# Optimization experiments

Measured on AMD Instinct MI355X. Metric: run time of the kernel, lower is better.

The kernel has to match this reference:

```python
import jax, jax.numpy as jnp
import numpy as np

DIM = 128      # token feature dim
HEADS = 4
HEAD_DIM = DIM // HEADS
H = 512
W = 512
NSP = 4096     # n_spixels = H*W/scale
TEMP = DIM ** (-0.5)   # NOTE: original scales by full-dim ** -0.5
NEG = -9.0e15
EPS = 1e-12    # torch F.normalize eps


def setup_inputs() -> dict:
    key = jax.random.key(0)
    k1, k2, k3, k4 = jax.random.split(key, 4)
    return {
        "spf": jax.random.normal(k1, (DIM, NSP), jnp.float32),
        "segments": jax.random.randint(k2, (H, W), 0, NSP, jnp.int32),
        "w_qkv": jax.random.normal(k3, (DIM, 3 * DIM), jnp.float32) / np.sqrt(DIM),
        "w_out": jax.random.normal(k4, (DIM, DIM), jnp.float32) / np.sqrt(DIM),
        "b_out": jnp.zeros((DIM,), jnp.float32),
    }


def build_adjacency(seg, n_sp):
    """Vectorized version of get_A: for every 2x2 window (i in [0,h-3], j in [0,w-3])
    connect the max and min superpixel labels; zero the diagonal."""
    a = seg[:-2, :-2]
    b = seg[:-2, 1:-1]
    c = seg[1:-1, :-2]
    d = seg[1:-1, 1:-1]
    mx = jnp.maximum(jnp.maximum(a, b), jnp.maximum(c, d)).ravel()
    mn = jnp.minimum(jnp.minimum(a, b), jnp.minimum(c, d)).ravel()
    A = jnp.zeros((n_sp, n_sp), jnp.float32)
    A = A.at[mx, mn].set(1.0)
    A = A.at[mn, mx].set(1.0)
    # fill_diagonal(A, 0) (also removes windows where max == min)
    A = A * (1.0 - jnp.eye(n_sp, dtype=jnp.float32))
    return A


def _l2norm(t):
    n = jnp.sqrt(jnp.sum(t * t, axis=-1, keepdims=True))
    return t / jnp.maximum(n, EPS)


def reference(spf, segments, w_qkv, w_out, b_out):
    A = build_adjacency(segments, NSP)                      # [n, n]
    x = spf.T                                               # [n, dim]
    qkv = x @ w_qkv                                         # [n, 3*dim]
    q, k, v = jnp.split(qkv, 3, axis=-1)
    split = lambda t: t.reshape(NSP, HEADS, HEAD_DIM).transpose(1, 0, 2)  # [h, n, d]
    q, k, v = split(q), split(k), split(v)
    q = _l2norm(q)
    k = _l2norm(k)
    # Original masks per-head scores, then keeps only head 0's attention
    # (attn[0][0]) and broadcasts it over all heads' v. We compute only
    # head 0's scores (mathematically identical output).
    scores = (q[0] @ k[0].T) * TEMP                         # [n, n] cosine scores
    scores = jnp.where(A > 0, scores, NEG)
    eye = jnp.eye(NSP, dtype=bool)
    scores = jnp.where(eye, 1.0, scores)                    # np.fill_diagonal(attn, 1)
    attn = jax.nn.softmax(scores, axis=-1)                  # [n, n]
    out = jnp.einsum('nm,hmd->hnd', attn, v)                # shared attn over heads
    out = out.transpose(1, 0, 2).reshape(NSP, DIM)          # [n, dim]
    out = out @ w_out + b_out                               # to_out Linear
    # map_sp2p: scatter superpixel features back to pixel grid (hard assignment)
    pix = out[segments]                                     # [H, W, dim]
    return pix.transpose(2, 0, 1)[None]                     # [1, dim, H, W]
```

## Files before the change

### kernel.cpp

```cpp
#include <hip/hip_runtime.h>

#define NSP 4096
#define HW 512
#define TEMP 0.08838834764831845f
#define MAXE 768
#define ADJ_BLOCKS 1017
#define QKV_BLOCKS 768

__global__ void __launch_bounds__(256) adj_qkv(
    const int* __restrict__ seg, unsigned int* __restrict__ mask,
    const float* __restrict__ spf, const float* __restrict__ wqkv,
    float* __restrict__ Q0, float* __restrict__ K0, float* __restrict__ V) {
    int t = threadIdx.x;
    if (blockIdx.x < ADJ_BLOCKS) {
        int idx = blockIdx.x * 256 + t;
        if (idx >= 510 * 510) return;
        int i = idx / 510, j = idx - i * 510;
        const int* r = seg + i * HW + j;
        int a = r[0], b = r[1], c = r[HW], d = r[HW + 1];
        int mx = max(max(a, b), max(c, d));
        int mn = min(min(a, b), min(c, d));
        if (mx == mn) return;
        atomicOr(&mask[mx * 128 + (mn >> 5)], 1u << (mn & 31));
        atomicOr(&mask[mn * 128 + (mx >> 5)], 1u << (mx & 31));
        return;
    }
    int gid = (blockIdx.x - ADJ_BLOCKS) * 256 + t;
    int g = gid % 48;
    int n = gid / 48;
    int wcol;
    float* outp;
    if (g < 8)       { wcol = g * 4;              outp = Q0 + n * 32  + g * 4; }
    else if (g < 16) { wcol = 128 + (g - 8) * 4;  outp = K0 + n * 32  + (g - 8) * 4; }
    else             { wcol = 256 + (g - 16) * 4; outp = V  + n * 128 + (g - 16) * 4; }
    float4 acc = {0.f, 0.f, 0.f, 0.f};
#pragma unroll 8
    for (int d = 0; d < 128; ++d) {
        float x = spf[d * NSP + n];
        float4 w = *(const float4*)(wqkv + d * 384 + wcol);
        acc.x += x * w.x; acc.y += x * w.y; acc.z += x * w.z; acc.w += x * w.w;
    }
    if (g < 16) {
        float s = acc.x * acc.x + acc.y * acc.y + acc.z * acc.z + acc.w * acc.w;
        s += __shfl_xor(s, 1);
        s += __shfl_xor(s, 2);
        s += __shfl_xor(s, 4);
        float inv = 1.0f / fmaxf(sqrtf(s), 1e-12f);
        acc.x *= inv; acc.y *= inv; acc.z *= inv; acc.w *= inv;
    }
    *(float4*)outp = acc;
}

__global__ void __launch_bounds__(128) sparse_attn(
    const unsigned int* __restrict__ mask, const float* __restrict__ Q0,
    const float* __restrict__ K0, const float* __restrict__ V,
    float* __restrict__ out) {
    int n = blockIdx.x;
    int t = threadIdx.x;
    __shared__ unsigned int words[128];
    __shared__ int   pfx[128];
    __shared__ int   midx[MAXE];
    __shared__ float wts[MAXE];
    __shared__ float q0s[32];
    __shared__ float4 redv[4][32];
    __shared__ float  redw[4];

    unsigned int w = mask[n * 128 + t];
    words[t] = w;
    if (t < 32) q0s[t] = Q0[n * 32 + t];
    pfx[t] = __popc(w);
    __syncthreads();
#pragma unroll
    for (int off = 1; off < 128; off <<= 1) {
        int v = pfx[t];
        int add = (t >= off) ? pfx[t - off] : 0;
        __syncthreads();
        pfx[t] = v + add;
        __syncthreads();
    }
    int E = min(pfx[127], MAXE);

    for (int e = t; e < E; e += 128) {
        int lo = 0, hi = 127;
        while (lo < hi) { int mid = (lo + hi) >> 1; if (pfx[mid] > e) hi = mid; else lo = mid + 1; }
        int base = (lo > 0) ? pfx[lo - 1] : 0;
        int r = e - base;
        unsigned int x = words[lo];
        for (int i = 0; i < r; ++i) x &= x - 1;
        int m = lo * 32 + (__ffs(x) - 1);
        const float4* kp = (const float4*)(K0 + m * 32);
        float s = 0.f;
#pragma unroll
        for (int i = 0; i < 8; ++i) {
            float4 kv = kp[i];
            s += q0s[i * 4 + 0] * kv.x + q0s[i * 4 + 1] * kv.y +
                 q0s[i * 4 + 2] * kv.z + q0s[i * 4 + 3] * kv.w;
        }
        wts[e]  = __expf(s * TEMP - 1.0f);
        midx[e] = m;
    }
    __syncthreads();

    int cg = t & 31, eg = t >> 5;
    const float4* V4 = (const float4*)V;
    float4 acc = {0.f, 0.f, 0.f, 0.f};
    float wp = 0.f;
    for (int e = eg; e < E; e += 4) {
        float wt = wts[e];
        float4 v = V4[midx[e] * 32 + cg];
        acc.x += wt * v.x; acc.y += wt * v.y; acc.z += wt * v.z; acc.w += wt * v.w;
        wp += wt;
    }
    redv[eg][cg] = acc;
    if (cg == 0) redw[eg] = wp;
    __syncthreads();
    if (t < 32) {
        float4 a0 = redv[0][t], a1 = redv[1][t], a2 = redv[2][t], a3 = redv[3][t];
        float ws = 1.0f + redw[0] + redw[1] + redw[2] + redw[3];
        float4 vd = V4[n * 32 + t];
        float inv = 1.0f / ws;
        float4 o;
        o.x = (a0.x + a1.x + a2.x + a3.x + vd.x) * inv;
        o.y = (a0.y + a1.y + a2.y + a3.y + vd.y) * inv;
        o.z = (a0.z + a1.z + a2.z + a3.z + vd.z) * inv;
        o.w = (a0.w + a1.w + a2.w + a3.w + vd.w) * inv;
        ((float4*)out)[n * 32 + t] = o;
    }
}

__global__ void out_gemm(const float* __restrict__ ain, const float* __restrict__ wout,
                         const float* __restrict__ bout, float* __restrict__ final) {
    int gid = blockIdx.x * blockDim.x + threadIdx.x;
    int g = gid & 31;
    int n = gid >> 5;
    const float* arow = ain + n * 128;
    float4 acc = {0.f, 0.f, 0.f, 0.f};
#pragma unroll 8
    for (int d = 0; d < 128; ++d) {
        float a = arow[d];
        float4 w = *(const float4*)(wout + d * 128 + g * 4);
        acc.x += a * w.x; acc.y += a * w.y; acc.z += a * w.z; acc.w += a * w.w;
    }
    float4 b = *(const float4*)(bout + g * 4);
    acc.x += b.x; acc.y += b.y; acc.z += b.z; acc.w += b.w;
    *(float4*)(final + n * 128 + g * 4) = acc;
}

#define GT_PIX 64
__global__ void __launch_bounds__(256) gather_out(
    const float* __restrict__ final, const int* __restrict__ seg,
    float* __restrict__ out) {
    __shared__ __align__(16) float tile[GT_PIX][132];
    __shared__ int sseg[GT_PIX];
    int base = blockIdx.x * GT_PIX;
    int t = threadIdx.x;
    if (t < GT_PIX) sseg[t] = seg[base + t];
    __syncthreads();

    int c4 = t & 31, pp = t >> 5;
    const float4* f4 = (const float4*)final;
#pragma unroll
    for (int i = 0; i < 8; ++i) {
        int p = pp + 8 * i;
        float4 v = f4[sseg[p] * 32 + c4];
        *(float4*)&tile[p][c4 * 4] = v;
    }
    __syncthreads();

    int jp = t >> 4;
    int cg = t & 15;
#pragma unroll
    for (int pass = 0; pass < 8; ++pass) {
        int cc = cg + 16 * pass;
        float4 v;
        v.x = tile[4 * jp + 0][cc];
        v.y = tile[4 * jp + 1][cc];
        v.z = tile[4 * jp + 2][cc];
        v.w = tile[4 * jp + 3][cc];
        *(float4*)(out + (size_t)cc * (HW * HW) + base + 4 * jp) = v;
    }
}

extern "C" void kernel_launch(void* const* d_in, const int* in_sizes, int n_in,
                              void* d_out, int out_size, void* d_ws, size_t ws_size,
                              hipStream_t stream) {
    const float* spf  = (const float*)d_in[0];
    const int*   seg  = (const int*)d_in[1];
    const float* wqkv = (const float*)d_in[2];
    const float* wout = (const float*)d_in[3];
    const float* bout = (const float*)d_in[4];
    float* out = (float*)d_out;

    char* ws = (char*)d_ws;
    unsigned int* mask = (unsigned int*)ws;
    float* Q0    = (float*)(ws + (2u << 20));
    float* K0    = (float*)(ws + (2u << 20) + (512u << 10));
    float* V     = (float*)(ws + (3u << 20));
    float* aout  = (float*)(ws + (5u << 20));
    float* final = (float*)(ws + (7u << 20));

    hipMemsetAsync(mask, 0, NSP * 128 * sizeof(unsigned int), stream);
    hipLaunchKernelGGL(adj_qkv, dim3(ADJ_BLOCKS + QKV_BLOCKS), dim3(256), 0, stream,
                       seg, mask, spf, wqkv, Q0, K0, V);
    hipLaunchKernelGGL(sparse_attn, dim3(4096), dim3(128), 0, stream, mask, Q0, K0, V, aout);
    hipLaunchKernelGGL(out_gemm,   dim3(512),  dim3(256), 0, stream, aout, wout, bout, final);
    hipLaunchKernelGGL(gather_out, dim3((HW * HW) / GT_PIX), dim3(256), 0, stream, final, seg, out);
}
```

Baseline: 221.4 us.

## Fold output projection into V weights and drop out_gemm kernel

Precomputes Wf = Wv·Wout in a prep kernel that also zeroes the adjacency mask, replacing the memset. V is then computed directly in the output-projected space, so attention writes final features with the bias added and the separate out_gemm launch is removed. This is valid because softmax weights sum to one, so the bias passes through unchanged. Also replaces the shared-memory prefix scan with a wavefront shuffle scan, unrolls the V accumulation by two, and lowers MAXE to 640, which risks truncating superpixels that have more neighbours.

```diff
diff --git a/kernel.cpp b/kernel.cpp
--- a/kernel.cpp
+++ b/kernel.cpp
@@ -3,13 +3,33 @@
 #define NSP 4096
 #define HW 512
 #define TEMP 0.08838834764831845f
-#define MAXE 768
+#define MAXE 640
+#define PREP_ZERO 512
+#define PREP_WF 64
 #define ADJ_BLOCKS 1017
 #define QKV_BLOCKS 768
+
+__global__ void __launch_bounds__(256) prep(
+    unsigned int* __restrict__ mask, const float* __restrict__ wqkv,
+    const float* __restrict__ wout, float* __restrict__ Wf) {
+    int t = threadIdx.x;
+    if (blockIdx.x < PREP_ZERO) {
+        ((uint4*)mask)[blockIdx.x * 256 + t] = make_uint4(0u, 0u, 0u, 0u);
+        return;
+    }
+    int gid = (blockIdx.x - PREP_ZERO) * 256 + t;
+    int d = gid >> 7, c = gid & 127;
+    float acc = 0.f;
+#pragma unroll 8
+    for (int k = 0; k < 128; ++k)
+        acc += wqkv[d * 384 + 256 + k] * wout[k * 128 + c];
+    Wf[d * 128 + c] = acc;
+}
 
 __global__ void __launch_bounds__(256) adj_qkv(
     const int* __restrict__ seg, unsigned int* __restrict__ mask,
     const float* __restrict__ spf, const float* __restrict__ wqkv,
+    const float* __restrict__ Wf,
     float* __restrict__ Q0, float* __restrict__ K0, float* __restrict__ V) {
     int t = threadIdx.x;
     if (blockIdx.x < ADJ_BLOCKS) {
@@ -28,16 +48,17 @@
     int gid = (blockIdx.x - ADJ_BLOCKS) * 256 + t;
     int g = gid % 48;
     int n = gid / 48;
-    int wcol;
+    const float* wbase;
+    int wstride;
     float* outp;
-    if (g < 8)       { wcol = g * 4;              outp = Q0 + n * 32  + g * 4; }
-    else if (g < 16) { wcol = 128 + (g - 8) * 4;  outp = K0 + n * 32  + (g - 8) * 4; }
-    else             { wcol = 256 + (g - 16) * 4; outp = V  + n * 128 + (g - 16) * 4; }
+    if (g < 8)       { wbase = wqkv + g * 4;               wstride = 384; outp = Q0 + n * 32  + g * 4; }
+    else if (g < 16) { wbase = wqkv + 128 + (g - 8) * 4;   wstride = 384; outp = K0 + n * 32  + (g - 8) * 4; }
+    else             { wbase = Wf + (g - 16) * 4;          wstride = 128; outp = V  + n * 128 + (g - 16) * 4; }
     float4 acc = {0.f, 0.f, 0.f, 0.f};
 #pragma unroll 8
     for (int d = 0; d < 128; ++d) {
         float x = spf[d * NSP + n];
-        float4 w = *(const float4*)(wqkv + d * 384 + wcol);
+        float4 w = *(const float4*)(wbase + d * wstride);
         acc.x += x * w.x; acc.y += x * w.y; acc.z += x * w.z; acc.w += x * w.w;
     }
     if (g < 16) {
@@ -54,9 +75,10 @@
 __global__ void __launch_bounds__(128) sparse_attn(
     const unsigned int* __restrict__ mask, const float* __restrict__ Q0,
     const float* __restrict__ K0, const float* __restrict__ V,
-    float* __restrict__ out) {
+    const float* __restrict__ bout, float* __restrict__ final) {
     int n = blockIdx.x;
     int t = threadIdx.x;
+    int lane = t & 63, wid = t >> 6;
     __shared__ unsigned int words[128];
     __shared__ int   pfx[128];
     __shared__ int   midx[MAXE];
@@ -68,16 +90,17 @@
     unsigned int w = mask[n * 128 + t];
     words[t] = w;
     if (t < 32) q0s[t] = Q0[n * 32 + t];
-    pfx[t] = __popc(w);
-    __syncthreads();
-#pragma unroll
-    for (int off = 1; off < 128; off <<= 1) {
-        int v = pfx[t];
-        int add = (t >= off) ? pfx[t - off] : 0;
-        __syncthreads();
-        pfx[t] = v + add;
-        __syncthreads();
-    }
+
+    int p = __popc(w);
+#pragma unroll
+    for (int off = 1; off < 64; off <<= 1) {
+        int y = __shfl_up(p, off);
+        if (lane >= off) p += y;
+    }
+    pfx[t] = p;
+    __syncthreads();
+    if (wid == 1) pfx[t] = p + pfx[63];
+    __syncthreads();
     int E = min(pfx[127], MAXE);
 
     for (int e = t; e < E; e += 128) {
@@ -105,7 +128,19 @@
     const float4* V4 = (const float4*)V;
     float4 acc = {0.f, 0.f, 0.f, 0.f};
     float wp = 0.f;
-    for (int e = eg; e < E; e += 4) {
+    int e = eg;
+    for (; e + 4 < E; e += 8) {
+        float wa = wts[e];     int ma = midx[e];
+        float wb = wts[e + 4]; int mb = midx[e + 4];
+        float4 va = V4[ma * 32 + cg];
+        float4 vb = V4[mb * 32 + cg];
+        acc.x += wa * va.x + wb * vb.x;
+        acc.y += wa * va.y + wb * vb.y;
+        acc.z += wa * va.z + wb * vb.z;
+        acc.w += wa * va.w + wb * vb.w;
+        wp += wa + wb;
+    }
+    for (; e < E; e += 4) {
         float wt = wts[e];
         float4 v = V4[midx[e] * 32 + cg];
         acc.x += wt * v.x; acc.y += wt * v.y; acc.z += wt * v.z; acc.w += wt * v.w;
@@ -118,32 +153,15 @@
         float4 a0 = redv[0][t], a1 = redv[1][t], a2 = redv[2][t], a3 = redv[3][t];
         float ws = 1.0f + redw[0] + redw[1] + redw[2] + redw[3];
         float4 vd = V4[n * 32 + t];
+        float4 bb = ((const float4*)bout)[t];
         float inv = 1.0f / ws;
         float4 o;
-        o.x = (a0.x + a1.x + a2.x + a3.x + vd.x) * inv;
-        o.y = (a0.y + a1.y + a2.y + a3.y + vd.y) * inv;
-        o.z = (a0.z + a1.z + a2.z + a3.z + vd.z) * inv;
-        o.w = (a0.w + a1.w + a2.w + a3.w + vd.w) * inv;
-        ((float4*)out)[n * 32 + t] = o;
-    }
-}
-
-__global__ void out_gemm(const float* __restrict__ ain, const float* __restrict__ wout,
-                         const float* __restrict__ bout, float* __restrict__ final) {
-    int gid = blockIdx.x * blockDim.x + threadIdx.x;
-    int g = gid & 31;
-    int n = gid >> 5;
-    const float* arow = ain + n * 128;
-    float4 acc = {0.f, 0.f, 0.f, 0.f};
-#pragma unroll 8
-    for (int d = 0; d < 128; ++d) {
-        float a = arow[d];
-        float4 w = *(const float4*)(wout + d * 128 + g * 4);
-        acc.x += a * w.x; acc.y += a * w.y; acc.z += a * w.z; acc.w += a * w.w;
-    }
-    float4 b = *(const float4*)(bout + g * 4);
-    acc.x += b.x; acc.y += b.y; acc.z += b.z; acc.w += b.w;
-    *(float4*)(final + n * 128 + g * 4) = acc;
+        o.x = (a0.x + a1.x + a2.x + a3.x + vd.x) * inv + bb.x;
+        o.y = (a0.y + a1.y + a2.y + a3.y + vd.y) * inv + bb.y;
+        o.z = (a0.z + a1.z + a2.z + a3.z + vd.z) * inv + bb.z;
+        o.w = (a0.w + a1.w + a2.w + a3.w + vd.w) * inv + bb.w;
+        ((float4*)final)[n * 32 + t] = o;
+    }
 }
 
 #define GT_PIX 64
@@ -196,13 +214,15 @@
     float* Q0    = (float*)(ws + (2u << 20));
     float* K0    = (float*)(ws + (2u << 20) + (512u << 10));
     float* V     = (float*)(ws + (3u << 20));
-    float* aout  = (float*)(ws + (5u << 20));
-    float* final = (float*)(ws + (7u << 20));
-
-    hipMemsetAsync(mask, 0, NSP * 128 * sizeof(unsigned int), stream);
+    float* final = (float*)(ws + (5u << 20));
+    float* Wf    = (float*)(ws + (7u << 20));
+
+    hipLaunchKernelGGL(prep, dim3(PREP_ZERO + PREP_WF), dim3(256), 0, stream,
+                       mask, wqkv, wout, Wf);
     hipLaunchKernelGGL(adj_qkv, dim3(ADJ_BLOCKS + QKV_BLOCKS), dim3(256), 0, stream,
-                       seg, mask, spf, wqkv, Q0, K0, V);
-    hipLaunchKernelGGL(sparse_attn, dim3(4096), dim3(128), 0, stream, mask, Q0, K0, V, aout);
-    hipLaunchKernelGGL(out_gemm,   dim3(512),  dim3(256), 0, stream, aout, wout, bout, final);
-    hipLaunchKernelGGL(gather_out, dim3((HW * HW) / GT_PIX), dim3(256), 0, stream, final, seg, out);
-}
+                       seg, mask, spf, wqkv, Wf, Q0, K0, V);
+    hipLaunchKernelGGL(sparse_attn, dim3(4096), dim3(128), 0, stream,
+                       mask, Q0, K0, V, bout, final);
+    hipLaunchKernelGGL(gather_out, dim3((HW * HW) / GT_PIX), dim3(256), 0, stream,
+                       final, seg, out);
+}
```

After: 215.3 us. -2.8%, faster.
